# Optimization experiments

Hardware: AMD Instinct MI355X
Metric: run time of the kernel (lower is better)

Reference implementation:

```python
import jax, jax.numpy as jnp
import numpy as np


def rotate_half(x):
    d = x.shape[-1] // 2
    return jnp.concatenate([-x[..., d:], x[..., :d]], axis=-1)


def setup_inputs() -> dict:
    key = jax.random.key(0)
    ks = jax.random.split(key, 8)
    B, T, C, H = 2, 2048, 2048, 16
    hd = C // H
    x = jax.random.normal(ks[0], (B, T, C), dtype=jnp.float32)
    # realistic RoPE tables
    inv_freq = 1.0 / (10000.0 ** (jnp.arange(0, hd, 2, dtype=jnp.float32) / hd))
    t = jnp.arange(T, dtype=jnp.float32)
    freqs = jnp.einsum('t,f->tf', t, inv_freq)
    emb = jnp.concatenate([freqs, freqs], axis=-1)  # [T, hd]
    cos = jnp.cos(emb)
    sin = jnp.sin(emb)
    mask = jnp.tril(jnp.ones((T, T), dtype=bool))[None, None]  # causal [1,1,T,T]
    s = C ** -0.5
    Wq = jax.random.normal(ks[1], (C, C), dtype=jnp.float32) * s
    Wk = jax.random.normal(ks[2], (C, C), dtype=jnp.float32) * s
    Wv = jax.random.normal(ks[3], (C, C), dtype=jnp.float32) * s
    Wo = jax.random.normal(ks[4], (C, C), dtype=jnp.float32) * s
    return {"x": x, "cos": cos, "sin": sin, "mask": mask,
            "Wq": Wq, "Wk": Wk, "Wv": Wv, "Wo": Wo}


def reference(x, cos, sin, mask, Wq, Wk, Wv, Wo):
    B, T, C = x.shape
    H = 16
    hd = C // H
    scale = hd ** -0.5
    # projections: torch Linear stores W as [out,in], y = x @ W^T
    def proj(W):
        return jnp.einsum('btc,dc->btd', x, W).reshape(B, T, H, hd).transpose(0, 2, 1, 3)
    q, k, v = proj(Wq), proj(Wk), proj(Wv)  # [B,H,T,hd]
    c = cos[None, None]  # [1,1,T,hd]
    s = sin[None, None]
    q = q * c + rotate_half(q) * s
    k = k * c + rotate_half(k) * s
    attn = jnp.einsum('bhqd,bhkd->bhqk', q, k) * scale
    attn = jnp.where(mask, attn, -jnp.inf)
    attn = jax.nn.softmax(attn, axis=-1)
    out = jnp.einsum('bhqk,bhkd->bhqd', attn, v)
    out = out.transpose(0, 2, 1, 3).reshape(B, T, C)
    return jnp.einsum('btc,dc->btd', out, Wo)
```

## Files before the change

kernel.cpp:

```cpp
#include <hip/hip_runtime.h>
#include <cstdint>

typedef __bf16 bf16_t;
typedef __bf16 bf16x8 __attribute__((ext_vector_type(8)));
typedef __bf16 bf16x4 __attribute__((ext_vector_type(4)));
typedef float  f32x4  __attribute__((ext_vector_type(4)));

#define BB 2
#define TT 2048
#define CC 2048
#define HH 16
#define HD 128

static __device__ __forceinline__ void async_copy16(const void* gp, void* lp) {
  __builtin_amdgcn_global_load_lds(
      (const __attribute__((address_space(1))) void*)(uintptr_t)gp,
      (__attribute__((address_space(3))) void*)(uint32_t)(uintptr_t)lp,
      16, 0, 0);
}

__global__ __launch_bounds__(256)
void cast_all(const float* __restrict__ x, const float* __restrict__ wq,
              const float* __restrict__ wk, const float* __restrict__ wv,
              const float* __restrict__ wo, bf16_t* __restrict__ xb,
              bf16_t* __restrict__ wq_b) {
  const int NX4 = (BB * TT * CC) / 4;
  const int NW4 = (CC * CC) / 4;
  int i = blockIdx.x * 256 + threadIdx.x;
  const float* s;
  bf16_t* d;
  int off;
  if (i < NX4) {
    s = x; d = xb; off = i;
  } else {
    int j = i - NX4;
    int w = j >> 20;
    off = j & (NW4 - 1);
    s = (w == 0) ? wq : (w == 1) ? wk : (w == 2) ? wv : wo;
    d = wq_b + (size_t)w * (CC * CC);
  }
  float4 v = ((const float4*)s)[off];
  bf16x4 o;
  o[0] = (bf16_t)v.x; o[1] = (bf16_t)v.y; o[2] = (bf16_t)v.z; o[3] = (bf16_t)v.w;
  ((bf16x4*)d)[off] = o;
}

template <int MODE>
__global__ __launch_bounds__(256)
void gemm_bt(const bf16_t* __restrict__ A, const bf16_t* __restrict__ Bw,
             void* __restrict__ C0, void* __restrict__ C1, void* __restrict__ C2,
             int Kdim, int Ndim) {
  __shared__ __align__(16) char smem[128 * 136 * 2];
  bf16_t* As = (bf16_t*)smem;
  bf16_t* Bs = (bf16_t*)(smem + 16384);
  const int tid  = threadIdx.x;
  const int wave = tid >> 6, lane = tid & 63;
  const int quad = lane >> 4, l16 = lane & 15;
  const int m0 = blockIdx.y * 128, n0 = blockIdx.x * 128;
  const int wm = (wave >> 1) * 64, wn = (wave & 1) * 64;

  f32x4 acc[4][4] = {};

  const int srow = lane >> 3;
  const int scol = (((lane & 7) ^ srow) & 7) * 8;
  const int swz  = (l16 & 7) * 8;

  for (int k0 = 0; k0 < Kdim; k0 += 64) {
#pragma unroll
    for (int i = 0; i < 4; ++i) {
      int chunk = wave * 4 + i;
      int row = chunk * 8 + srow;
      async_copy16(A + (size_t)(m0 + row) * Kdim + k0 + scol, As + chunk * 512);
    }
#pragma unroll
    for (int i = 0; i < 4; ++i) {
      int chunk = wave * 4 + i;
      int row = chunk * 8 + srow;
      async_copy16(Bw + (size_t)(n0 + row) * Kdim + k0 + scol, Bs + chunk * 512);
    }
    __syncthreads();
#pragma unroll
    for (int kk = 0; kk < 64; kk += 32) {
      const int koff = (kk + quad * 8) ^ swz;
      bf16x8 af[4], bfr[4];
#pragma unroll
      for (int i = 0; i < 4; ++i)
        af[i] = *(const bf16x8*)&As[(wm + i * 16 + l16) * 64 + koff];
#pragma unroll
      for (int j = 0; j < 4; ++j)
        bfr[j] = *(const bf16x8*)&Bs[(wn + j * 16 + l16) * 64 + koff];
#pragma unroll
      for (int i = 0; i < 4; ++i)
#pragma unroll
        for (int j = 0; j < 4; ++j)
          acc[i][j] = __builtin_amdgcn_mfma_f32_16x16x32_bf16(af[i], bfr[j], acc[i][j], 0, 0, 0);
    }
    __syncthreads();
  }

#pragma unroll
  for (int i = 0; i < 4; ++i)
#pragma unroll
    for (int j = 0; j < 4; ++j) {
      int gcol = n0 + wn + j * 16 + l16;
#pragma unroll
      for (int r = 0; r < 4; ++r) {
        int grow = m0 + wm + i * 16 + quad * 4 + r;
        ((float*)C0)[(size_t)grow * Ndim + gcol] = acc[i][j][r];
      }
    }
}

__global__ __launch_bounds__(512, 2)
void gemm_qkv256(const bf16_t* __restrict__ A, const bf16_t* __restrict__ Bw,
                 bf16_t* __restrict__ Qo, bf16_t* __restrict__ Ko,
                 bf16_t* __restrict__ Vo, int Kdim) {
  extern __shared__ __align__(16) char smem[];
  bf16_t* lds = (bf16_t*)smem;
  const int tid  = threadIdx.x;
  const int wave = tid >> 6, lane = tid & 63;
  const int quad = lane >> 4, l16 = lane & 15;
  const int wm = wave >> 2, wn = wave & 3;
  const int n0 = blockIdx.x * 256, m0 = blockIdx.y * 256;

  const int srow = lane >> 3;
  const int scol = ((lane & 7) ^ srow) * 8;
  const int swz  = (l16 & 7) * 8;
  const int nK = Kdim >> 6;

  const bf16_t* Ag = A  + (size_t)(m0 + wave * 32 + srow) * Kdim + scol;
  const bf16_t* Bg = Bw + (size_t)(n0 + wave * 32 + srow) * Kdim + scol;
  const int ldsChunk = wave * 4 * 512;

#define STAGE_A(kt, buf)                                                      \
  {                                                                           \
    bf16_t* dstA = lds + (buf) * 32768 + ldsChunk;                            \
    const bf16_t* srcA = Ag + (kt) * 64;                                      \
    _Pragma("unroll")                                                         \
    for (int ci = 0; ci < 4; ++ci)                                            \
      async_copy16(srcA + (size_t)(ci * 8) * Kdim, dstA + ci * 512);          \
  }
#define STAGE_B(kt, buf)                                                      \
  {                                                                           \
    bf16_t* dstB = lds + (buf) * 32768 + 16384 + ldsChunk;                    \
    const bf16_t* srcB = Bg + (kt) * 64;                                      \
    _Pragma("unroll")                                                         \
    for (int ci = 0; ci < 4; ++ci)                                            \
      async_copy16(srcB + (size_t)(ci * 8) * Kdim, dstB + ci * 512);          \
  }

  f32x4 acc[8][4] = {};

  STAGE_A(0, 0); STAGE_B(0, 0); STAGE_A(1, 1); STAGE_B(1, 1);

  const int k0off = (quad * 8) ^ swz;
  const int k1off = (32 + quad * 8) ^ swz;

  for (int k = 0; k < nK; ++k) {
    const int cur = k & 1;
    const bf16_t* Asb = lds + cur * 32768;
    const bf16_t* Bsb = Asb + 16384;
    if (k < nK - 1) asm volatile("s_waitcnt vmcnt(8)" ::: "memory");
    else            asm volatile("s_waitcnt vmcnt(0)" ::: "memory");
    __builtin_amdgcn_s_barrier();
    __builtin_amdgcn_sched_barrier(0);

    bf16x8 a0[8], b0[4], a1[8], b1[4];
#pragma unroll
    for (int i = 0; i < 8; ++i)
      a0[i] = *(const bf16x8*)&Asb[(wm * 128 + i * 16 + l16) * 64 + k0off];
#pragma unroll
    for (int j = 0; j < 4; ++j)
      b0[j] = *(const bf16x8*)&Bsb[(wn * 64 + j * 16 + l16) * 64 + k0off];
    asm volatile("s_waitcnt lgkmcnt(0)" ::: "memory");
    __builtin_amdgcn_sched_barrier(0);
    __builtin_amdgcn_s_setprio(1);
#pragma unroll
    for (int i = 0; i < 4; ++i)
#pragma unroll
      for (int j = 0; j < 4; ++j)
        acc[i][j] = __builtin_amdgcn_mfma_f32_16x16x32_bf16(a0[i], b0[j], acc[i][j], 0, 0, 0);
    __builtin_amdgcn_s_setprio(0);

#pragma unroll
    for (int i = 0; i < 8; ++i)
      a1[i] = *(const bf16x8*)&Asb[(wm * 128 + i * 16 + l16) * 64 + k1off];
#pragma unroll
    for (int j = 0; j < 4; ++j)
      b1[j] = *(const bf16x8*)&Bsb[(wn * 64 + j * 16 + l16) * 64 + k1off];
    __builtin_amdgcn_s_setprio(1);
#pragma unroll
    for (int i = 4; i < 8; ++i)
#pragma unroll
      for (int j = 0; j < 4; ++j)
        acc[i][j] = __builtin_amdgcn_mfma_f32_16x16x32_bf16(a0[i], b0[j], acc[i][j], 0, 0, 0);
    __builtin_amdgcn_s_setprio(0);
    asm volatile("s_waitcnt lgkmcnt(0)" ::: "memory");
    __builtin_amdgcn_s_barrier();
    __builtin_amdgcn_sched_barrier(0);

    if (k + 2 < nK) STAGE_A(k + 2, cur);
    __builtin_amdgcn_s_setprio(1);
#pragma unroll
    for (int i = 0; i < 4; ++i)
#pragma unroll
      for (int j = 0; j < 4; ++j)
        acc[i][j] = __builtin_amdgcn_mfma_f32_16x16x32_bf16(a1[i], b1[j], acc[i][j], 0, 0, 0);
    __builtin_amdgcn_s_setprio(0);

    if (k + 2 < nK) STAGE_B(k + 2, cur);
    __builtin_amdgcn_s_setprio(1);
#pragma unroll
    for (int i = 4; i < 8; ++i)
#pragma unroll
      for (int j = 0; j < 4; ++j)
        acc[i][j] = __builtin_amdgcn_mfma_f32_16x16x32_bf16(a1[i], b1[j], acc[i][j], 0, 0, 0);
    __builtin_amdgcn_s_setprio(0);
  }
#undef STAGE_A
#undef STAGE_B

  const int proj = n0 >> 11;
  if (proj < 2) {
    bf16_t* dst = proj == 0 ? Qo : Ko;
#pragma unroll
    for (int i = 0; i < 8; ++i)
#pragma unroll
      for (int j = 0; j < 4; ++j) {
        int colv = (n0 & (CC - 1)) + wn * 64 + j * 16 + l16;
        int h = colv >> 7, d = colv & (HD - 1);
#pragma unroll
        for (int r = 0; r < 4; ++r) {
          int grow = m0 + wm * 128 + i * 16 + quad * 4 + r;
          int b = grow >> 11, t = grow & (TT - 1);
          dst[(((size_t)(b * HH + h) * TT + t) * HD) + d] = (bf16_t)acc[i][j][r];
        }
      }
  } else {
    bf16_t* Ct = (bf16_t*)smem;
    const int b = m0 >> 11;
#pragma unroll
    for (int p = 0; p < 2; ++p) {
      __syncthreads();
      if (wm == p) {
#pragma unroll
        for (int i = 0; i < 8; ++i)
#pragma unroll
          for (int j = 0; j < 4; ++j) {
            int c = wn * 64 + j * 16 + l16;
#pragma unroll
            for (int r = 0; r < 4; ++r)
              Ct[(i * 16 + quad * 4 + r) * 264 + c] = (bf16_t)acc[i][j][r];
          }
      }
      __syncthreads();
      const unsigned short* Cu = (const unsigned short*)Ct;
      int c  = tid & 255;
      int rh = (tid >> 8) * 64;
      int dv = (n0 & (CC - 1)) + c;
      int h = dv >> 7, d = dv & (HD - 1);
      unsigned int pk[32];
#pragma unroll
      for (int s = 0; s < 32; ++s) {
        unsigned int lo = Cu[(rh + 2 * s) * 264 + c];
        unsigned int hi = Cu[(rh + 2 * s + 1) * 264 + c];
        pk[s] = lo | (hi << 16);
      }
      bf16_t* dstp = Vo + ((size_t)(b * HH + h) * HD + d) * TT +
                     (m0 & (TT - 1)) + p * 128 + rh;
#pragma unroll
      for (int u = 0; u < 8; ++u) {
        uint4 w; w.x = pk[4*u]; w.y = pk[4*u+1]; w.z = pk[4*u+2]; w.w = pk[4*u+3];
        *(uint4*)(dstp + 8 * u) = w;
      }
    }
  }
}

__global__ __launch_bounds__(256) void rope_kernel(bf16_t* __restrict__ Q, bf16_t* __restrict__ K,
                                                   const float* __restrict__ cosT,
                                                   const float* __restrict__ sinT) {
  int idx = blockIdx.x * 256 + threadIdx.x;
  int d  = idx & 63;
  int t  = (idx >> 6) & (TT - 1);
  int bh = idx >> 17;
  size_t base = ((size_t)bh * TT + t) * HD;
  float c0 = cosT[t * HD + d],      s0 = sinT[t * HD + d];
  float c1 = cosT[t * HD + 64 + d], s1 = sinT[t * HD + 64 + d];
  float q0 = Q[base + d], q1 = Q[base + 64 + d];
  Q[base + d]      = (bf16_t)(q0 * c0 - q1 * s0);
  Q[base + 64 + d] = (bf16_t)(q1 * c1 + q0 * s1);
  float k0 = K[base + d], k1 = K[base + 64 + d];
  K[base + d]      = (bf16_t)(k0 * c0 - k1 * s0);
  K[base + 64 + d] = (bf16_t)(k1 * c1 + k0 * s1);
}

__global__ __launch_bounds__(256)
void attn_kernel(const bf16_t* __restrict__ Q, const bf16_t* __restrict__ K,
                 const bf16_t* __restrict__ Vt, bf16_t* __restrict__ Out) {
  __shared__ __align__(16) bf16_t Ks[2][64 * 128];
  __shared__ __align__(16) bf16_t Vs[2][128 * 64];
  __shared__ __align__(16) bf16_t Pl[4][2][16 * 72];
  const int lane = threadIdx.x & 63, wave = threadIdx.x >> 6;
  const int quad = lane >> 4, l16 = lane & 15;
  const int linear = blockIdx.x;
  const int hb = linear & 31;
  const int h = hb & (HH - 1), b = hb >> 4;
  const int qt = (TT / 128 - 1) - (linear >> 5);
  const int q0 = qt * 128 + wave * 32;
  const size_t qkbase = (size_t)(b * HH + h) * TT * HD;
  const bf16_t* Kh = K + qkbase;
  const bf16_t* Vh = Vt + (size_t)(b * HH + h) * HD * TT;
  const float scale = 0.08838834764831845f;

  const int srK = lane >> 4;
  const int sgK = lane & 15;
  const int scK0 = (sgK ^ srK) * 8;
  const int scK1 = (sgK ^ (4 + srK)) * 8;
  const int srV = lane >> 3;
  const int scV = (((lane & 7) ^ srV) & 7) * 8;
  const int swz = (l16 & 7) * 8;

  bf16x8 qf[2][4];
#pragma unroll
  for (int mt = 0; mt < 2; ++mt) {
    const bf16_t* qrow = Q + qkbase + (size_t)(q0 + mt * 16 + l16) * HD;
#pragma unroll
    for (int kc = 0; kc < 4; ++kc) qf[mt][kc] = *(const bf16x8*)(qrow + kc * 32 + quad * 8);
  }

  f32x4 o[2][8] = {};
  float l_i[2][4] = {};

  const int nIter = qt * 2 + 2;

  {
#pragma unroll
    for (int i = 0; i < 4; ++i) {
      int chunk = wave * 4 + i;
      int sc = (chunk & 1) ? scK1 : scK0;
      async_copy16(Kh + (size_t)(chunk * 4 + srK) * HD + sc, &Ks[0][chunk * 512]);
    }
#pragma unroll
    for (int i = 0; i < 4; ++i) {
      int chunk = wave * 4 + i;
      async_copy16(Vh + (size_t)(chunk * 8 + srV) * TT + scV, &Vs[0][chunk * 512]);
    }
  }

  for (int it = 0; it < nIter; ++it) {
    const int cur = it & 1;
    const int key0 = it * 64;
    __syncthreads();

    if (it + 1 < nIter) {
      const int nxt = cur ^ 1;
      const int knxt = key0 + 64;
#pragma unroll
      for (int i = 0; i < 4; ++i) {
        int chunk = wave * 4 + i;
        int sc = (chunk & 1) ? scK1 : scK0;
        async_copy16(Kh + (size_t)(knxt + chunk * 4 + srK) * HD + sc, &Ks[nxt][chunk * 512]);
      }
#pragma unroll
      for (int i = 0; i < 4; ++i) {
        int chunk = wave * 4 + i;
        async_copy16(Vh + (size_t)(chunk * 8 + srV) * TT + knxt + scV, &Vs[nxt][chunk * 512]);
      }
    }

    f32x4 s[2][4] = {};
#pragma unroll
    for (int kc = 0; kc < 4; ++kc) {
      const int koff = (kc * 32 + quad * 8) ^ swz;
#pragma unroll
      for (int kt = 0; kt < 4; ++kt) {
        bf16x8 kf = *(const bf16x8*)&Ks[cur][(kt * 16 + l16) * 128 + koff];
        s[0][kt] = __builtin_amdgcn_mfma_f32_16x16x32_bf16(qf[0][kc], kf, s[0][kt], 0, 0, 0);
        s[1][kt] = __builtin_amdgcn_mfma_f32_16x16x32_bf16(qf[1][kc], kf, s[1][kt], 0, 0, 0);
      }
    }

#pragma unroll
    for (int mt = 0; mt < 2; ++mt) {
      bf16_t* pl = &Pl[wave][mt][0];
#pragma unroll
      for (int r = 0; r < 4; ++r) {
        int rel = q0 + mt * 16 + quad * 4 + r - key0;
        int prow = (quad * 4 + r) * 72;
        float lr = 0.f;
#pragma unroll
        for (int kt = 0; kt < 4; ++kt) {
          int c16 = kt * 16 + l16;
          float e = (c16 > rel) ? 0.f : __expf(s[mt][kt][r] * scale);
          lr += e;
          pl[prow + c16] = (bf16_t)e;
        }
        l_i[mt][r] += lr;
      }
    }

    bf16x8 pf[2][2];
#pragma unroll
    for (int mt = 0; mt < 2; ++mt) {
      pf[mt][0] = *(const bf16x8*)&Pl[wave][mt][l16 * 72 + quad * 8];
      pf[mt][1] = *(const bf16x8*)&Pl[wave][mt][l16 * 72 + 32 + quad * 8];
    }
    const int voff0 = (quad * 8) ^ swz;
    const int voff1 = (32 + quad * 8) ^ swz;
#pragma unroll
    for (int n = 0; n < 8; ++n) {
      bf16x8 vf0 = *(const bf16x8*)&Vs[cur][(n * 16 + l16) * 64 + voff0];
      bf16x8 vf1 = *(const bf16x8*)&Vs[cur][(n * 16 + l16) * 64 + voff1];
      o[0][n] = __builtin_amdgcn_mfma_f32_16x16x32_bf16(pf[0][0], vf0, o[0][n], 0, 0, 0);
      o[0][n] = __builtin_amdgcn_mfma_f32_16x16x32_bf16(pf[0][1], vf1, o[0][n], 0, 0, 0);
      o[1][n] = __builtin_amdgcn_mfma_f32_16x16x32_bf16(pf[1][0], vf0, o[1][n], 0, 0, 0);
      o[1][n] = __builtin_amdgcn_mfma_f32_16x16x32_bf16(pf[1][1], vf1, o[1][n], 0, 0, 0);
    }
  }

#pragma unroll
  for (int mt = 0; mt < 2; ++mt)
#pragma unroll
    for (int r = 0; r < 4; ++r) {
      float l = l_i[mt][r];
#pragma unroll
      for (int off = 1; off < 16; off <<= 1) l += __shfl_xor(l, off);
      l_i[mt][r] = 1.f / l;
    }

#pragma unroll
  for (int mt = 0; mt < 2; ++mt)
#pragma unroll
    for (int n = 0; n < 8; ++n)
#pragma unroll
      for (int r = 0; r < 4; ++r) {
        int qg = q0 + mt * 16 + quad * 4 + r;
        size_t off = ((size_t)(b * TT + qg) * CC) + h * HD + n * 16 + l16;
        Out[off] = (bf16_t)(o[mt][n][r] * l_i[mt][r]);
      }
}

extern "C" void kernel_launch(void* const* d_in, const int* in_sizes, int n_in,
                              void* d_out, int out_size, void* d_ws, size_t ws_size,
                              hipStream_t stream) {
  const float* x    = (const float*)d_in[0];
  const float* cosT = (const float*)d_in[1];
  const float* sinT = (const float*)d_in[2];
  const float* Wq = (const float*)d_in[4];
  const float* Wk = (const float*)d_in[5];
  const float* Wv = (const float*)d_in[6];
  const float* Wo = (const float*)d_in[7];
  float* out = (float*)d_out;

  char* ws = (char*)d_ws;
  const size_t XSZ = (size_t)BB * TT * CC * 2;
  const size_t WSZ = (size_t)CC * CC * 2;
  bf16_t* x_bf  = (bf16_t*)(ws);
  bf16_t* wq_bf = (bf16_t*)(ws + XSZ);
  bf16_t* wo_bf = (bf16_t*)(ws + XSZ + 3 * WSZ);
  bf16_t* Qb    = (bf16_t*)(ws + XSZ + 4 * WSZ);
  bf16_t* Kb    = (bf16_t*)(ws + 2 * XSZ + 4 * WSZ);
  bf16_t* Vt    = (bf16_t*)(ws + 3 * XSZ + 4 * WSZ);
  bf16_t* attn_bf = x_bf;

  const int NX = BB * TT * CC;
  const int NW = CC * CC;
  cast_all<<<(NX / 4 + 4 * (NW / 4)) / 256, 256, 0, stream>>>(
      x, Wq, Wk, Wv, Wo, x_bf, wq_bf);

  (void)hipFuncSetAttribute(reinterpret_cast<const void*>(gemm_qkv256),
                            hipFuncAttributeMaxDynamicSharedMemorySize, 131072);
  gemm_qkv256<<<dim3(3 * CC / 256, BB * TT / 256), 512, 131072, stream>>>(
      x_bf, wq_bf, Qb, Kb, Vt, CC);

  rope_kernel<<<(BB * HH * TT * 64) / 256, 256, 0, stream>>>(Qb, Kb, cosT, sinT);

  attn_kernel<<<dim3(BB * HH * (TT / 128)), 256, 0, stream>>>(Qb, Kb, Vt, attn_bf);

  gemm_bt<0><<<dim3(CC / 128, BB * TT / 128), 256, 0, stream>>>(
      attn_bf, wo_bf, out, nullptr, nullptr, CC, CC);
}
```

Measured before the change: 383.8 us.

## Pair causal query tiles per block and widen attention blocks to 8 waves

Each attention block now runs with 512 threads, and each wave owns 16 query rows instead of 32. The block processes two query tiles in sequence, one from the heavy end and one from the light end (15-spair and spair), so every block does the same total causal work. This removes load imbalance and tail effects in the grid and lowers register pressure per wave, which allows 2 blocks per CU. In exchange, each K/V tile loaded into LDS is reused by only 16 query rows per wave rather than 32, and there are half as many blocks (256), which lowers parallelism at the grid level.

Result: faster. 375.0 us (-2.3%).

```diff
diff --git a/kernel.cpp b/kernel.cpp
--- a/kernel.cpp
+++ b/kernel.cpp
@@ -295,19 +295,18 @@
   K[base + 64 + d] = (bf16_t)(k1 * c1 + k0 * s1);
 }
 
-__global__ __launch_bounds__(256)
+__global__ __launch_bounds__(512, 2)
 void attn_kernel(const bf16_t* __restrict__ Q, const bf16_t* __restrict__ K,
                  const bf16_t* __restrict__ Vt, bf16_t* __restrict__ Out) {
   __shared__ __align__(16) bf16_t Ks[2][64 * 128];
   __shared__ __align__(16) bf16_t Vs[2][128 * 64];
-  __shared__ __align__(16) bf16_t Pl[4][2][16 * 72];
+  __shared__ __align__(16) bf16_t Pl[8][16 * 72];
   const int lane = threadIdx.x & 63, wave = threadIdx.x >> 6;
   const int quad = lane >> 4, l16 = lane & 15;
   const int linear = blockIdx.x;
   const int hb = linear & 31;
   const int h = hb & (HH - 1), b = hb >> 4;
-  const int qt = (TT / 128 - 1) - (linear >> 5);
-  const int q0 = qt * 128 + wave * 32;
+  const int spair = linear >> 5;
   const size_t qkbase = (size_t)(b * HH + h) * TT * HD;
   const bf16_t* Kh = K + qkbase;
   const bf16_t* Vh = Vt + (size_t)(b * HH + h) * HD * TT;
@@ -321,124 +320,116 @@
   const int scV = (((lane & 7) ^ srV) & 7) * 8;
   const int swz = (l16 & 7) * 8;
 
-  bf16x8 qf[2][4];
-#pragma unroll
-  for (int mt = 0; mt < 2; ++mt) {
-    const bf16_t* qrow = Q + qkbase + (size_t)(q0 + mt * 16 + l16) * HD;
-#pragma unroll
-    for (int kc = 0; kc < 4; ++kc) qf[mt][kc] = *(const bf16x8*)(qrow + kc * 32 + quad * 8);
-  }
-
-  f32x4 o[2][8] = {};
-  float l_i[2][4] = {};
-
-  const int nIter = qt * 2 + 2;
-
-  {
-#pragma unroll
-    for (int i = 0; i < 4; ++i) {
-      int chunk = wave * 4 + i;
-      int sc = (chunk & 1) ? scK1 : scK0;
-      async_copy16(Kh + (size_t)(chunk * 4 + srK) * HD + sc, &Ks[0][chunk * 512]);
-    }
-#pragma unroll
-    for (int i = 0; i < 4; ++i) {
-      int chunk = wave * 4 + i;
-      async_copy16(Vh + (size_t)(chunk * 8 + srV) * TT + scV, &Vs[0][chunk * 512]);
-    }
-  }
-
-  for (int it = 0; it < nIter; ++it) {
-    const int cur = it & 1;
-    const int key0 = it * 64;
-    __syncthreads();
-
-    if (it + 1 < nIter) {
-      const int nxt = cur ^ 1;
-      const int knxt = key0 + 64;
-#pragma unroll
-      for (int i = 0; i < 4; ++i) {
-        int chunk = wave * 4 + i;
+#pragma unroll
+  for (int half = 0; half < 2; ++half) {
+    const int qt = half == 0 ? (15 - spair) : spair;
+    const int q0 = qt * 128 + wave * 16;
+    const int nIter = qt * 2 + 2;
+
+    bf16x8 qf[4];
+    {
+      const bf16_t* qrow = Q + qkbase + (size_t)(q0 + l16) * HD;
+#pragma unroll
+      for (int kc = 0; kc < 4; ++kc) qf[kc] = *(const bf16x8*)(qrow + kc * 32 + quad * 8);
+    }
+
+    f32x4 o[8] = {};
+    float l_i[4] = {};
+
+    {
+#pragma unroll
+      for (int i = 0; i < 2; ++i) {
+        int chunk = wave * 2 + i;
         int sc = (chunk & 1) ? scK1 : scK0;
-        async_copy16(Kh + (size_t)(knxt + chunk * 4 + srK) * HD + sc, &Ks[nxt][chunk * 512]);
-      }
-#pragma unroll
-      for (int i = 0; i < 4; ++i) {
-        int chunk = wave * 4 + i;
-        async_copy16(Vh + (size_t)(chunk * 8 + srV) * TT + knxt + scV, &Vs[nxt][chunk * 512]);
-      }
-    }
-
-    f32x4 s[2][4] = {};
-#pragma unroll
-    for (int kc = 0; kc < 4; ++kc) {
-      const int koff = (kc * 32 + quad * 8) ^ swz;
-#pragma unroll
-      for (int kt = 0; kt < 4; ++kt) {
-        bf16x8 kf = *(const bf16x8*)&Ks[cur][(kt * 16 + l16) * 128 + koff];
-        s[0][kt] = __builtin_amdgcn_mfma_f32_16x16x32_bf16(qf[0][kc], kf, s[0][kt], 0, 0, 0);
-        s[1][kt] = __builtin_amdgcn_mfma_f32_16x16x32_bf16(qf[1][kc], kf, s[1][kt], 0, 0, 0);
-      }
-    }
-
-#pragma unroll
-    for (int mt = 0; mt < 2; ++mt) {
-      bf16_t* pl = &Pl[wave][mt][0];
+        async_copy16(Kh + (size_t)(chunk * 4 + srK) * HD + sc, &Ks[0][chunk * 512]);
+      }
+#pragma unroll
+      for (int i = 0; i < 2; ++i) {
+        int chunk = wave * 2 + i;
+        async_copy16(Vh + (size_t)(chunk * 8 + srV) * TT + scV, &Vs[0][chunk * 512]);
+      }
+    }
+
+    for (int it = 0; it < nIter; ++it) {
+      const int cur = it & 1;
+      const int key0 = it * 64;
+      __syncthreads();
+
+      if (it + 1 < nIter) {
+        const int nxt = cur ^ 1;
+        const int knxt = key0 + 64;
+#pragma unroll
+        for (int i = 0; i < 2; ++i) {
+          int chunk = wave * 2 + i;
+          int sc = (chunk & 1) ? scK1 : scK0;
+          async_copy16(Kh + (size_t)(knxt + chunk * 4 + srK) * HD + sc, &Ks[nxt][chunk * 512]);
+        }
+#pragma unroll
+        for (int i = 0; i < 2; ++i) {
+          int chunk = wave * 2 + i;
+          async_copy16(Vh + (size_t)(chunk * 8 + srV) * TT + knxt + scV, &Vs[nxt][chunk * 512]);
+        }
+      }
+
+      f32x4 s[4] = {};
+#pragma unroll
+      for (int kc = 0; kc < 4; ++kc) {
+        const int koff = (kc * 32 + quad * 8) ^ swz;
+#pragma unroll
+        for (int kt = 0; kt < 4; ++kt) {
+          bf16x8 kf = *(const bf16x8*)&Ks[cur][(kt * 16 + l16) * 128 + koff];
+          s[kt] = __builtin_amdgcn_mfma_f32_16x16x32_bf16(qf[kc], kf, s[kt], 0, 0, 0);
+        }
+      }
+
+      {
+        bf16_t* pl = &Pl[wave][0];
+#pragma unroll
+        for (int r = 0; r < 4; ++r) {
+          int rel = q0 + quad * 4 + r - key0;
+          int prow = (quad * 4 + r) * 72;
+          float lr = 0.f;
+#pragma unroll
+          for (int kt = 0; kt < 4; ++kt) {
+            int c16 = kt * 16 + l16;
+            float e = (c16 > rel) ? 0.f : __expf(s[kt][r] * scale);
+            lr += e;
+            pl[prow + c16] = (bf16_t)e;
+          }
+          l_i[r] += lr;
+        }
+      }
+
+      bf16x8 pf0 = *(const bf16x8*)&Pl[wave][l16 * 72 + quad * 8];
+      bf16x8 pf1 = *(const bf16x8*)&Pl[wave][l16 * 72 + 32 + quad * 8];
+      const int voff0 = (quad * 8) ^ swz;
+      const int voff1 = (32 + quad * 8) ^ swz;
+#pragma unroll
+      for (int n = 0; n < 8; ++n) {
+        bf16x8 vf0 = *(const bf16x8*)&Vs[cur][(n * 16 + l16) * 64 + voff0];
+        bf16x8 vf1 = *(const bf16x8*)&Vs[cur][(n * 16 + l16) * 64 + voff1];
+        o[n] = __builtin_amdgcn_mfma_f32_16x16x32_bf16(pf0, vf0, o[n], 0, 0, 0);
+        o[n] = __builtin_amdgcn_mfma_f32_16x16x32_bf16(pf1, vf1, o[n], 0, 0, 0);
+      }
+    }
+
+#pragma unroll
+    for (int r = 0; r < 4; ++r) {
+      float l = l_i[r];
+#pragma unroll
+      for (int off = 1; off < 16; off <<= 1) l += __shfl_xor(l, off);
+      l_i[r] = 1.f / l;
+    }
+
+#pragma unroll
+    for (int n = 0; n < 8; ++n)
 #pragma unroll
       for (int r = 0; r < 4; ++r) {
-        int rel = q0 + mt * 16 + quad * 4 + r - key0;
-        int prow = (quad * 4 + r) * 72;
-        float lr = 0.f;
-#pragma unroll
-        for (int kt = 0; kt < 4; ++kt) {
-          int c16 = kt * 16 + l16;
-          float e = (c16 > rel) ? 0.f : __expf(s[mt][kt][r] * scale);
-          lr += e;
-          pl[prow + c16] = (bf16_t)e;
-        }
-        l_i[mt][r] += lr;
-      }
-    }
-
-    bf16x8 pf[2][2];
-#pragma unroll
-    for (int mt = 0; mt < 2; ++mt) {
-      pf[mt][0] = *(const bf16x8*)&Pl[wave][mt][l16 * 72 + quad * 8];
-      pf[mt][1] = *(const bf16x8*)&Pl[wave][mt][l16 * 72 + 32 + quad * 8];
-    }
-    const int voff0 = (quad * 8) ^ swz;
-    const int voff1 = (32 + quad * 8) ^ swz;
-#pragma unroll
-    for (int n = 0; n < 8; ++n) {
-      bf16x8 vf0 = *(const bf16x8*)&Vs[cur][(n * 16 + l16) * 64 + voff0];
-      bf16x8 vf1 = *(const bf16x8*)&Vs[cur][(n * 16 + l16) * 64 + voff1];
-      o[0][n] = __builtin_amdgcn_mfma_f32_16x16x32_bf16(pf[0][0], vf0, o[0][n], 0, 0, 0);
-      o[0][n] = __builtin_amdgcn_mfma_f32_16x16x32_bf16(pf[0][1], vf1, o[0][n], 0, 0, 0);
-      o[1][n] = __builtin_amdgcn_mfma_f32_16x16x32_bf16(pf[1][0], vf0, o[1][n], 0, 0, 0);
-      o[1][n] = __builtin_amdgcn_mfma_f32_16x16x32_bf16(pf[1][1], vf1, o[1][n], 0, 0, 0);
-    }
-  }
-
-#pragma unroll
-  for (int mt = 0; mt < 2; ++mt)
-#pragma unroll
-    for (int r = 0; r < 4; ++r) {
-      float l = l_i[mt][r];
-#pragma unroll
-      for (int off = 1; off < 16; off <<= 1) l += __shfl_xor(l, off);
-      l_i[mt][r] = 1.f / l;
-    }
-
-#pragma unroll
-  for (int mt = 0; mt < 2; ++mt)
-#pragma unroll
-    for (int n = 0; n < 8; ++n)
-#pragma unroll
-      for (int r = 0; r < 4; ++r) {
-        int qg = q0 + mt * 16 + quad * 4 + r;
+        int qg = q0 + quad * 4 + r;
         size_t off = ((size_t)(b * TT + qg) * CC) + h * HD + n * 16 + l16;
-        Out[off] = (bf16_t)(o[mt][n][r] * l_i[mt][r]);
-      }
+        Out[off] = (bf16_t)(o[n][r] * l_i[r]);
+      }
+  }
 }
 
 extern "C" void kernel_launch(void* const* d_in, const int* in_sizes, int n_in,
@@ -476,7 +467,7 @@
 
   rope_kernel<<<(BB * HH * TT * 64) / 256, 256, 0, stream>>>(Qb, Kb, cosT, sinT);
 
-  attn_kernel<<<dim3(BB * HH * (TT / 128)), 256, 0, stream>>>(Qb, Kb, Vt, attn_bf);
+  attn_kernel<<<dim3(BB * HH * 8), 512, 0, stream>>>(Qb, Kb, Vt, attn_bf);
 
   gemm_bt<0><<<dim3(CC / 128, BB * TT / 128), 256, 0, stream>>>(
       attn_bf, wo_bf, out, nullptr, nullptr, CC, CC);
```
